# Performance work log

Measured on AMD Instinct MI355X. Metric: run time of the kernel, lower is better.

## Reference

```python
import jax, jax.numpy as jnp
import numpy as np

T = 20          # num_time_steps
THR = 0.05      # IafPscDelta threshold (and latency-encoding threshold)
REF = 3         # refractory_time_steps
DAMP = 1.0      # dampening_factor for surrogate gradient

@jax.custom_vjp
def spike(v_scaled):
    return (v_scaled > 0.0).astype(v_scaled.dtype)

def _spike_fwd(v_scaled):
    return spike(v_scaled), v_scaled

def _spike_bwd(v_scaled, g):
    # triangular surrogate: damp * max(0, 1 - |v_scaled|)
    return (g * DAMP * jnp.maximum(0.0, 1.0 - jnp.abs(v_scaled)),)

spike.defvjp(_spike_fwd, _spike_bwd)

def latency_encode(x):
    # snntorch.spikegen.latency(..., tau=2, threshold=0.05, normalize=True, linear=True, clip=True)
    # normalize+linear => spike_time = (T-1)*(1-x), clamped at (T-1)*(1-thr)
    tau_eff = jnp.asarray(T - 1, x.dtype)
    st = jnp.minimum(tau_eff * (1.0 - x), tau_eff * (1.0 - THR))
    t_idx = jnp.clip(jnp.round(st), 0, T - 1).astype(jnp.int32)          # [B,1,28,28]
    mask = (x >= THR).astype(x.dtype)                                     # clip=True: no spike if x < thr
    steps = jnp.arange(T, dtype=jnp.int32).reshape(T, 1, 1, 1, 1)
    return (steps == t_idx[None]).astype(x.dtype) * mask[None]            # [T,B,1,28,28]

def conv_all_steps(frames, W):
    # frames: [T,B,C,H,W]; shared weights -> batch the conv over T*B frames
    Tt, B, C, H, Wsp = frames.shape
    y = jax.lax.conv_general_dilated(frames.reshape(Tt * B, C, H, Wsp), W,
                                     window_strides=(1, 1), padding='SAME',
                                     dimension_numbers=('NCHW', 'OIHW', 'NCHW'))
    return y.reshape(Tt, B, W.shape[0], H, Wsp)

def lif(seq):
    # IafPscDelta over time: integrate (no leak), threshold, soft reset, refractory
    # seq: [T, B, ...] input currents per step
    v0 = jnp.zeros_like(seq[0])
    r0 = jnp.zeros_like(seq[0])
    def step(carry, x_t):
        v, r = carry
        v = v + x_t
        z = spike((v - THR) / THR)
        z = jnp.where(r > 0.0, jnp.zeros_like(z), z)   # refractory suppresses spikes
        v = v - z * THR                                 # perfect_reset=False -> subtract thr
        r = jnp.where(z > 0.0, jnp.full_like(r, REF), jnp.maximum(r - 1.0, 0.0))
        return (v, r), z
    _, zs = jax.lax.scan(step, (v0, r0), seq)
    return zs

def maxpool2(seq):
    Tt, B, C, H, Wsp = seq.shape
    y = jax.lax.reduce_window(seq.reshape(Tt * B, C, H, Wsp), 0.0, jax.lax.max,
                              (1, 1, 2, 2), (1, 1, 2, 2), 'VALID')
    return y.reshape(Tt, B, C, H // 2, Wsp // 2)

def setup_inputs() -> dict:
    key = jax.random.key(0)
    k1, k2, k3, k4 = jax.random.split(key, 4)
    x = jax.random.uniform(k1, (128, 1, 28, 28), dtype=jnp.float32)
    W1 = jax.random.normal(k2, (32, 1, 3, 3), dtype=jnp.float32) / np.sqrt(1 * 9)
    W2 = jax.random.normal(k3, (32, 32, 3, 3), dtype=jnp.float32) / np.sqrt(32 * 9)
    Wd = jax.random.normal(k4, (64, 32 * 7 * 7), dtype=jnp.float32) / np.sqrt(32 * 7 * 7)
    return {"x": x, "W1": W1, "W2": W2, "Wd": Wd}

def reference(x, W1, W2, Wd):
    s = latency_encode(x)                       # [T,B,1,28,28]
    h = maxpool2(lif(conv_all_steps(s, W1)))    # [T,B,32,14,14]
    h = maxpool2(lif(conv_all_steps(h, W2)))    # [T,B,32,7,7]
    Tt, B = h.shape[0], h.shape[1]
    h = h.reshape(Tt, B, -1)                    # [T,B,1568]
    h = lif(jnp.einsum('tbf,of->tbo', h, Wd))   # [T,B,64] output spikes
    return jnp.transpose(h, (1, 0, 2))          # [B,T,64]
```

## Files before the change

kernel.cpp:

```cpp
#include <hip/hip_runtime.h>

#define THRF 0.05f

__global__ void k_encode_mask(const float* __restrict__ x, unsigned* __restrict__ m, int n) {
  int i = blockIdx.x * blockDim.x + threadIdx.x;
  if (i >= n) return;
  float xv = x[i];
  float st = fminf(19.0f * (1.0f - xv), 19.0f * 0.95f);
  int t = (int)rintf(st);
  t = t < 0 ? 0 : (t > 19 ? 19 : t);
  m[i] = (xv >= THRF) ? (1u << t) : 0u;
}

__global__ void k_wt(const float* __restrict__ W1, const float* __restrict__ W2,
                     const float* __restrict__ Wd, float* __restrict__ w1T,
                     float* __restrict__ w2T, float* __restrict__ WdT) {
  int i = blockIdx.x * blockDim.x + threadIdx.x;
  if (i < 288) { int oc = i / 9, k = i % 9; w1T[k * 32 + oc] = W1[i]; }
  if (i < 9216) {
    int oc = i / 288, k = i % 288, ic = k / 9, kk = k % 9;
    w2T[kk * 1024 + ic * 32 + oc] = W2[i];
  }
  if (i < 100352) { int o = i / 1568, f = i % 1568; WdT[f * 64 + o] = Wd[i]; }
}

__global__ __launch_bounds__(128) void k_stage1M(const unsigned* __restrict__ mIn,
                                                 const float* __restrict__ w1T,
                                                 unsigned* __restrict__ z1p) {
  __shared__ float xp[2][20 * 66];
  int lane = threadIdx.x & 63;
  int wid  = threadIdx.x >> 6;
  int gw   = blockIdx.x * 2 + wid;
  int pA = 2 * gw, pB = 2 * gw + 1;
  int bA = pA / 784, rA = pA % 784, yA = rA / 28, xA = rA % 28;
  int bB = pB / 784, rB = pB % 784, yB = rB / 28, xB = rB % 28;
  int tl = lane & 31, hiB = lane >> 5;

  unsigned mA[9], mB[9];
  for (int ky = 0; ky < 3; ++ky) {
    for (int kx = 0; kx < 3; ++kx) {
      int k = ky * 3 + kx;
      int ya = yA - 1 + ky, xa = xA - 1 + kx;
      int yb = yB - 1 + ky, xb = xB - 1 + kx;
      mA[k] = (ya >= 0 && ya < 28 && xa >= 0 && xa < 28) ? mIn[bA * 784 + ya * 28 + xa] : 0u;
      mB[k] = (yb >= 0 && yb < 28 && xb >= 0 && xb < 28) ? mIn[bB * 784 + yb * 28 + xb] : 0u;
    }
  }

  float acc[32];
#pragma unroll
  for (int o = 0; o < 32; ++o) acc[o] = 0.0f;

  for (int k = 0; k < 9; ++k) {
    unsigned long long m64 = ((unsigned long long)mB[k] << 32) | (unsigned long long)mA[k];
    float bitf = (float)((m64 >> lane) & 1ull);
    const float* wrow = w1T + k * 32;
#pragma unroll
    for (int oc = 0; oc < 32; ++oc)
      acc[oc] = fmaf(wrow[oc], bitf, acc[oc]);
  }

  if (tl < 20) {
#pragma unroll
    for (int oc = 0; oc < 32; ++oc)
      xp[wid][tl * 66 + hiB * 32 + oc] = acc[oc];
  }
  __syncthreads();

  float v = 0.0f;
  int   r = 0;
  unsigned zm = 0u;
#pragma unroll
  for (int t = 0; t < 20; ++t) {
    float c = xp[wid][t * 66 + lane];
    v += c;
    bool z = (v > THRF) && (r == 0);
    if (z) { v -= THRF; r = 3; } else if (r > 0) --r;
    if (z) zm |= 1u << t;
  }
  int p = hiB ? pB : pA;
  int b = p / 784, rr = p % 784, y = rr / 28, x = rr % 28;
  atomicOr(&z1p[((b * 14 + (y >> 1)) * 14 + (x >> 1)) * 32 + tl], zm);
}

__global__ __launch_bounds__(256) void k_stage2E(const unsigned* __restrict__ z1p,
                                                 const float* __restrict__ wT2,
                                                 const unsigned* __restrict__ zbuf,
                                                 unsigned* __restrict__ z2p) {
  __shared__ float xp[4][20 * 97];
  int lane = threadIdx.x & 63;
  int wid  = threadIdx.x >> 6;
  int gw   = blockIdx.x * 4 + wid;
  int q0 = 3 * gw, q1 = q0 + 1, q2 = q0 + 2;
  bool vq0 = q0 < 25088, vq1 = q1 < 25088, vq2 = q2 < 25088;
  int b0 = q0 / 196, r0 = q0 % 196, y0 = r0 / 14, x0 = r0 % 14;
  int b1 = q1 / 196, r1 = q1 % 196, y1 = r1 / 14, x1 = r1 % 14;
  int b2 = q2 / 196, r2 = q2 % 196, y2 = r2 / 14, x2 = r2 % 14;

  int  li = lane & 31;
  bool lo = lane < 32;
  int  p  = lane / 20;
  int  tl = lane - p * 20;

  float acc[32];
#pragma unroll
  for (int o = 0; o < 32; ++o) acc[o] = 0.0f;

  auto cptr = [&](int ky, int kx, const unsigned*& c0, const unsigned*& c1,
                  const unsigned*& c2) {
    int y0k = y0 - 1 + ky, y1k = y1 - 1 + ky, y2k = y2 - 1 + ky;
    int x0k = x0 - 1 + kx, x1k = x1 - 1 + kx, x2k = x2 - 1 + kx;
    bool ok0 = vq0 && y0k >= 0 && y0k < 14 && x0k >= 0 && x0k < 14;
    bool ok1 = vq1 && y1k >= 0 && y1k < 14 && x1k >= 0 && x1k < 14;
    bool ok2 = vq2 && y2k >= 0 && y2k < 14 && x2k >= 0 && x2k < 14;
    c0 = ok0 ? (z1p + ((b0 * 14 + y0k) * 14 + x0k) * 32) : zbuf;
    c1 = ok1 ? (z1p + ((b1 * 14 + y1k) * 14 + x1k) * 32) : zbuf;
    c2 = ok2 ? (z1p + ((b2 * 14 + y2k) * 14 + x2k) * 32) : zbuf;
  };

  const unsigned *c0, *c1, *c2;
  cptr(0, 0, c0, c1, c2);
  unsigned va = (lo ? c0 : c1)[li];
  unsigned vb = c2[li];

  for (int ky = 0; ky < 3; ++ky) {
    for (int kx = 0; kx < 3; ++kx) {
      unsigned va_n = 0u, vb_n = 0u;
      int nkx = kx + 1, nky = ky;
      if (nkx == 3) { nkx = 0; nky = ky + 1; }
      if (nky < 3) {
        const unsigned *n0, *n1, *n2;
        cptr(nky, nkx, n0, n1, n2);
        va_n = (lo ? n0 : n1)[li];
        vb_n = n2[li];
      }
      const float* wc = wT2 + (ky * 3 + kx) * 1024;
#pragma unroll
      for (int ic = 0; ic < 32; ++ic) {
        unsigned s0 = (unsigned)__builtin_amdgcn_readlane((int)va, ic);
        unsigned s1 = (unsigned)__builtin_amdgcn_readlane((int)va, 32 + ic);
        unsigned s2 = (unsigned)__builtin_amdgcn_readlane((int)vb, ic);
        unsigned mm = (p == 0) ? s0 : ((p == 1) ? s1 : s2);
        float bitf = (float)((mm >> tl) & 1u);
        const float* wrow = wc + ic * 32;
#pragma unroll
        for (int oc = 0; oc < 32; ++oc)
          acc[oc] = fmaf(wrow[oc], bitf, acc[oc]);
      }
      va = va_n; vb = vb_n;
    }
  }

  if (p < 3) {
#pragma unroll
    for (int oc = 0; oc < 32; ++oc)
      xp[wid][tl * 97 + p * 32 + oc] = acc[oc];
  }
  __syncthreads();

  for (int pass = 0; pass < 2; ++pass) {
    int n = lane + 64 * pass;
    if (n < 96) {
      int pp = n >> 5;
      int oc = n & 31;
      int q  = q0 + pp;
      if (q < 25088) {
        float v = 0.0f;
        int   r = 0;
        unsigned zm = 0u;
#pragma unroll
        for (int t = 0; t < 20; ++t) {
          float c = xp[wid][t * 97 + n];
          v += c;
          bool z = (v > THRF) && (r == 0);
          if (z) { v -= THRF; r = 3; } else if (r > 0) --r;
          if (z) zm |= 1u << t;
        }
        int b = q / 196, rr = q % 196, y = rr / 14, x = rr % 14;
        atomicOr(&z2p[b * 1568 + oc * 49 + (y >> 1) * 7 + (x >> 1)], zm);
      }
    }
  }
}

__global__ __launch_bounds__(256) void k_dense_curE(const unsigned* __restrict__ z2p,
                                                    const float* __restrict__ WdT,
                                                    float* __restrict__ cur) {
  int lane = threadIdx.x & 63;
  int wid  = threadIdx.x >> 6;
  int gw   = blockIdx.x * 4 + wid;
  if (gw >= 128 * 22) return;
  int b  = gw / 22, og = gw % 22;
  int p  = lane / 20;
  int t  = lane - p * 20;
  int o  = og * 3 + p;
  bool live = (p < 3) && (o < 64);
  int osafe = live ? o : 63;
  const unsigned* zb = z2p + b * 1568;

  unsigned mA[16], mB[16];
  float    wA[16], wB[16];
#pragma unroll
  for (int u = 0; u < 16; ++u) { mA[u] = zb[u]; wA[u] = WdT[u * 64 + osafe]; }

  float acc = 0.0f;
  for (int f0 = 0; f0 < 1568; f0 += 32) {
#pragma unroll
    for (int u = 0; u < 16; ++u) {
      int fn = f0 + 16 + u;
      mB[u] = zb[fn]; wB[u] = WdT[fn * 64 + osafe];
    }
#pragma unroll
    for (int u = 0; u < 16; ++u) {
      float bitf = (float)((mA[u] >> t) & 1u);
      acc = fmaf(wA[u], bitf, acc);
    }
    if (f0 + 32 < 1568) {
#pragma unroll
      for (int u = 0; u < 16; ++u) {
        int fn = f0 + 32 + u;
        mA[u] = zb[fn]; wA[u] = WdT[fn * 64 + osafe];
      }
    }
#pragma unroll
    for (int u = 0; u < 16; ++u) {
      float bitf = (float)((mB[u] >> t) & 1u);
      acc = fmaf(wB[u], bitf, acc);
    }
  }
  if (live) cur[(b * 64 + o) * 20 + t] = acc;
}

__global__ void k_dense_lif(const float* __restrict__ cur, float* __restrict__ out) {
  int idx = blockIdx.x * blockDim.x + threadIdx.x;
  if (idx >= 128 * 64) return;
  int o = idx % 64;
  int b = idx / 64;
  const float* c = cur + (b * 64 + o) * 20;
  float v = 0.0f;
  int   r = 0;
  for (int t = 0; t < 20; ++t) {
    v += c[t];
    bool z = (v > THRF) && (r == 0);
    if (z) { v -= THRF; r = 3; } else if (r > 0) --r;
    out[(b * 20 + t) * 64 + o] = z ? 1.0f : 0.0f;
  }
}

extern "C" void kernel_launch(void* const* d_in, const int* in_sizes, int n_in,
                              void* d_out, int out_size, void* d_ws, size_t ws_size,
                              hipStream_t stream) {
  const float* x  = (const float*)d_in[0];
  const float* W1 = (const float*)d_in[1];
  const float* W2 = (const float*)d_in[2];
  const float* Wd = (const float*)d_in[3];
  float* out = (float*)d_out;

  char* ws = (char*)d_ws;
  unsigned* mIn  = (unsigned*)ws;
  float*    cur  = (float*)ws;
  unsigned* z1p  = (unsigned*)(ws + 655360);
  unsigned* z2p  = (unsigned*)(ws + 3866624);
  unsigned* zbuf = (unsigned*)(ws + 4669440);
  float*    w1T  = (float*)(ws + 4669568);
  float*    w2T  = (float*)(ws + 4670720);
  float*    WdT  = (float*)(ws + 4707584);

  k_encode_mask<<<dim3(392), dim3(256), 0, stream>>>(x, mIn, 128 * 784);
  k_wt<<<dim3(392), dim3(256), 0, stream>>>(W1, W2, Wd, w1T, w2T, WdT);
  hipMemsetAsync(ws + 655360, 0, 3211264 + 802816 + 128, stream);
  k_stage1M<<<dim3(25088), dim3(128), 0, stream>>>(mIn, w1T, z1p);
  k_stage2E<<<dim3(2091), dim3(256), 0, stream>>>(z1p, w2T, zbuf, z2p);
  k_dense_curE<<<dim3(704), dim3(256), 0, stream>>>(z2p, WdT, cur);
  k_dense_lif<<<dim3(32), dim3(256), 0, stream>>>(cur, out);
}
```

Baseline: 279.5 us.

## Process six pixels per wave in conv2, fuse dense LIF, merge prep kernels

The stage-2 conv kernel now computes two groups of three pixels per wavefront. Each weight float4 load feeds two accumulator sets, and per-lane bit extraction uses a packed 64-bit mask instead of selects. The dense LIF is folded into the dense kernel through wave shuffles, which drops the intermediate current buffer and one launch. The encode and weight-transpose kernels are also merged into one. Together these halve weight traffic per pixel and cut launch overhead, at the cost of higher register pressure from 64 accumulators and a partial unroll of the ic loop.

```diff
diff --git a/kernel.cpp b/kernel.cpp
--- a/kernel.cpp
+++ b/kernel.cpp
@@ -2,26 +2,23 @@
 
 #define THRF 0.05f
 
-__global__ void k_encode_mask(const float* __restrict__ x, unsigned* __restrict__ m, int n) {
+__global__ void k_pre(const float* __restrict__ x, const float* __restrict__ W1,
+                      const float* __restrict__ W2, const float* __restrict__ Wd,
+                      unsigned* __restrict__ mIn, float* __restrict__ w1T,
+                      float* __restrict__ w2T, float* __restrict__ WdT) {
   int i = blockIdx.x * blockDim.x + threadIdx.x;
-  if (i >= n) return;
+  if (i >= 100352) return;
   float xv = x[i];
   float st = fminf(19.0f * (1.0f - xv), 19.0f * 0.95f);
   int t = (int)rintf(st);
   t = t < 0 ? 0 : (t > 19 ? 19 : t);
-  m[i] = (xv >= THRF) ? (1u << t) : 0u;
-}
-
-__global__ void k_wt(const float* __restrict__ W1, const float* __restrict__ W2,
-                     const float* __restrict__ Wd, float* __restrict__ w1T,
-                     float* __restrict__ w2T, float* __restrict__ WdT) {
-  int i = blockIdx.x * blockDim.x + threadIdx.x;
-  if (i < 288) { int oc = i / 9, k = i % 9; w1T[k * 32 + oc] = W1[i]; }
+  mIn[i] = (xv >= THRF) ? (1u << t) : 0u;
+  { int o = i / 1568, f = i % 1568; WdT[f * 64 + o] = Wd[i]; }
   if (i < 9216) {
     int oc = i / 288, k = i % 288, ic = k / 9, kk = k % 9;
     w2T[kk * 1024 + ic * 32 + oc] = W2[i];
   }
-  if (i < 100352) { int o = i / 1568, f = i % 1568; WdT[f * 64 + o] = Wd[i]; }
+  if (i < 288) { int oc = i / 9, k = i % 9; w1T[k * 32 + oc] = W1[i]; }
 }
 
 __global__ __launch_bounds__(128) void k_stage1M(const unsigned* __restrict__ mIn,
@@ -83,7 +80,7 @@
   atomicOr(&z1p[((b * 14 + (y >> 1)) * 14 + (x >> 1)) * 32 + tl], zm);
 }
 
-__global__ __launch_bounds__(256) void k_stage2E(const unsigned* __restrict__ z1p,
+__global__ __launch_bounds__(256) void k_stage2F(const unsigned* __restrict__ z1p,
                                                  const float* __restrict__ wT2,
                                                  const unsigned* __restrict__ zbuf,
                                                  unsigned* __restrict__ z2p) {
@@ -91,101 +88,110 @@
   int lane = threadIdx.x & 63;
   int wid  = threadIdx.x >> 6;
   int gw   = blockIdx.x * 4 + wid;
-  int q0 = 3 * gw, q1 = q0 + 1, q2 = q0 + 2;
-  bool vq0 = q0 < 25088, vq1 = q1 < 25088, vq2 = q2 < 25088;
-  int b0 = q0 / 196, r0 = q0 % 196, y0 = r0 / 14, x0 = r0 % 14;
-  int b1 = q1 / 196, r1 = q1 % 196, y1 = r1 / 14, x1 = r1 % 14;
-  int b2 = q2 / 196, r2 = q2 % 196, y2 = r2 / 14, x2 = r2 % 14;
-
+  int q0 = 6 * gw;
   int  li = lane & 31;
   bool lo = lane < 32;
   int  p  = lane / 20;
   int  tl = lane - p * 20;
 
-  float acc[32];
-#pragma unroll
-  for (int o = 0; o < 32; ++o) acc[o] = 0.0f;
-
-  auto cptr = [&](int ky, int kx, const unsigned*& c0, const unsigned*& c1,
-                  const unsigned*& c2) {
-    int y0k = y0 - 1 + ky, y1k = y1 - 1 + ky, y2k = y2 - 1 + ky;
-    int x0k = x0 - 1 + kx, x1k = x1 - 1 + kx, x2k = x2 - 1 + kx;
-    bool ok0 = vq0 && y0k >= 0 && y0k < 14 && x0k >= 0 && x0k < 14;
-    bool ok1 = vq1 && y1k >= 0 && y1k < 14 && x1k >= 0 && x1k < 14;
-    bool ok2 = vq2 && y2k >= 0 && y2k < 14 && x2k >= 0 && x2k < 14;
-    c0 = ok0 ? (z1p + ((b0 * 14 + y0k) * 14 + x0k) * 32) : zbuf;
-    c1 = ok1 ? (z1p + ((b1 * 14 + y1k) * 14 + x1k) * 32) : zbuf;
-    c2 = ok2 ? (z1p + ((b2 * 14 + y2k) * 14 + x2k) * 32) : zbuf;
-  };
-
-  const unsigned *c0, *c1, *c2;
-  cptr(0, 0, c0, c1, c2);
-  unsigned va = (lo ? c0 : c1)[li];
-  unsigned vb = c2[li];
+  int qq[6], bb[6], yy[6], xx[6];
+  bool vq[6];
+#pragma unroll
+  for (int j = 0; j < 6; ++j) {
+    int q = q0 + j;
+    qq[j] = q; vq[j] = q < 25088;
+    int qs = vq[j] ? q : 0;
+    bb[j] = qs / 196; int rr = qs % 196; yy[j] = rr / 14; xx[j] = rr % 14;
+  }
+
+  float accA[32], accB[32];
+#pragma unroll
+  for (int o = 0; o < 32; ++o) { accA[o] = 0.0f; accB[o] = 0.0f; }
 
   for (int ky = 0; ky < 3; ++ky) {
     for (int kx = 0; kx < 3; ++kx) {
-      unsigned va_n = 0u, vb_n = 0u;
-      int nkx = kx + 1, nky = ky;
-      if (nkx == 3) { nkx = 0; nky = ky + 1; }
-      if (nky < 3) {
-        const unsigned *n0, *n1, *n2;
-        cptr(nky, nkx, n0, n1, n2);
-        va_n = (lo ? n0 : n1)[li];
-        vb_n = n2[li];
-      }
+      const unsigned* cp[6];
+#pragma unroll
+      for (int j = 0; j < 6; ++j) {
+        int y = yy[j] - 1 + ky, x = xx[j] - 1 + kx;
+        bool ok = vq[j] && y >= 0 && y < 14 && x >= 0 && x < 14;
+        cp[j] = ok ? (z1p + ((bb[j] * 14 + y) * 14 + x) * 32) : zbuf;
+      }
+      unsigned vaA = (lo ? cp[0] : cp[1])[li];
+      unsigned vbA = cp[2][li];
+      unsigned vaB = (lo ? cp[3] : cp[4])[li];
+      unsigned vbB = cp[5][li];
       const float* wc = wT2 + (ky * 3 + kx) * 1024;
-#pragma unroll
+#pragma unroll 4
       for (int ic = 0; ic < 32; ++ic) {
-        unsigned s0 = (unsigned)__builtin_amdgcn_readlane((int)va, ic);
-        unsigned s1 = (unsigned)__builtin_amdgcn_readlane((int)va, 32 + ic);
-        unsigned s2 = (unsigned)__builtin_amdgcn_readlane((int)vb, ic);
-        unsigned mm = (p == 0) ? s0 : ((p == 1) ? s1 : s2);
-        float bitf = (float)((mm >> tl) & 1u);
-        const float* wrow = wc + ic * 32;
-#pragma unroll
-        for (int oc = 0; oc < 32; ++oc)
-          acc[oc] = fmaf(wrow[oc], bitf, acc[oc]);
-      }
-      va = va_n; vb = vb_n;
-    }
-  }
-
-  if (p < 3) {
-#pragma unroll
-    for (int oc = 0; oc < 32; ++oc)
-      xp[wid][tl * 97 + p * 32 + oc] = acc[oc];
-  }
-  __syncthreads();
-
-  for (int pass = 0; pass < 2; ++pass) {
-    int n = lane + 64 * pass;
-    if (n < 96) {
-      int pp = n >> 5;
-      int oc = n & 31;
-      int q  = q0 + pp;
-      if (q < 25088) {
-        float v = 0.0f;
-        int   r = 0;
-        unsigned zm = 0u;
-#pragma unroll
-        for (int t = 0; t < 20; ++t) {
-          float c = xp[wid][t * 97 + n];
-          v += c;
-          bool z = (v > THRF) && (r == 0);
-          if (z) { v -= THRF; r = 3; } else if (r > 0) --r;
-          if (z) zm |= 1u << t;
+        unsigned s0 = (unsigned)__builtin_amdgcn_readlane((int)vaA, ic);
+        unsigned s1 = (unsigned)__builtin_amdgcn_readlane((int)vaA, 32 + ic);
+        unsigned s2 = (unsigned)__builtin_amdgcn_readlane((int)vbA, ic);
+        unsigned s3 = (unsigned)__builtin_amdgcn_readlane((int)vaB, ic);
+        unsigned s4 = (unsigned)__builtin_amdgcn_readlane((int)vaB, 32 + ic);
+        unsigned s5 = (unsigned)__builtin_amdgcn_readlane((int)vbB, ic);
+        unsigned long long BA = (unsigned long long)s0 |
+                                ((unsigned long long)s1 << 20) |
+                                ((unsigned long long)s2 << 40);
+        unsigned long long BB = (unsigned long long)s3 |
+                                ((unsigned long long)s4 << 20) |
+                                ((unsigned long long)s5 << 40);
+        float bfA = (float)((BA >> lane) & 1ull);
+        float bfB = (float)((BB >> lane) & 1ull);
+        const float4* w4 = (const float4*)(wc + ic * 32);
+#pragma unroll
+        for (int j = 0; j < 8; ++j) {
+          float4 w = w4[j];
+          accA[4 * j + 0] = fmaf(w.x, bfA, accA[4 * j + 0]);
+          accA[4 * j + 1] = fmaf(w.y, bfA, accA[4 * j + 1]);
+          accA[4 * j + 2] = fmaf(w.z, bfA, accA[4 * j + 2]);
+          accA[4 * j + 3] = fmaf(w.w, bfA, accA[4 * j + 3]);
+          accB[4 * j + 0] = fmaf(w.x, bfB, accB[4 * j + 0]);
+          accB[4 * j + 1] = fmaf(w.y, bfB, accB[4 * j + 1]);
+          accB[4 * j + 2] = fmaf(w.z, bfB, accB[4 * j + 2]);
+          accB[4 * j + 3] = fmaf(w.w, bfB, accB[4 * j + 3]);
         }
-        int b = q / 196, rr = q % 196, y = rr / 14, x = rr % 14;
-        atomicOr(&z2p[b * 1568 + oc * 49 + (y >> 1) * 7 + (x >> 1)], zm);
-      }
-    }
-  }
-}
-
-__global__ __launch_bounds__(256) void k_dense_curE(const unsigned* __restrict__ z2p,
-                                                    const float* __restrict__ WdT,
-                                                    float* __restrict__ cur) {
+      }
+    }
+  }
+
+#pragma unroll
+  for (int s = 0; s < 2; ++s) {
+    if (p < 3) {
+#pragma unroll
+      for (int oc = 0; oc < 32; ++oc)
+        xp[wid][tl * 97 + p * 32 + oc] = (s == 0 ? accA[oc] : accB[oc]);
+    }
+    __syncthreads();
+    for (int pass = 0; pass < 2; ++pass) {
+      int n = lane + 64 * pass;
+      if (n < 96) {
+        int pp = n >> 5;
+        int oc = n & 31;
+        int j  = 3 * s + pp;
+        if (vq[j]) {
+          float v = 0.0f;
+          int   r = 0;
+          unsigned zm = 0u;
+#pragma unroll
+          for (int t = 0; t < 20; ++t) {
+            float c = xp[wid][t * 97 + n];
+            v += c;
+            bool z = (v > THRF) && (r == 0);
+            if (z) { v -= THRF; r = 3; } else if (r > 0) --r;
+            if (z) zm |= 1u << t;
+          }
+          atomicOr(&z2p[bb[j] * 1568 + oc * 49 + (yy[j] >> 1) * 7 + (xx[j] >> 1)], zm);
+        }
+      }
+    }
+    __syncthreads();
+  }
+}
+
+__global__ __launch_bounds__(256) void k_denseF(const unsigned* __restrict__ z2p,
+                                                const float* __restrict__ WdT,
+                                                float* __restrict__ out) {
   int lane = threadIdx.x & 63;
   int wid  = threadIdx.x >> 6;
   int gw   = blockIdx.x * 4 + wid;
@@ -228,23 +234,19 @@
       acc = fmaf(wB[u], bitf, acc);
     }
   }
-  if (live) cur[(b * 64 + o) * 20 + t] = acc;
-}
-
-__global__ void k_dense_lif(const float* __restrict__ cur, float* __restrict__ out) {
-  int idx = blockIdx.x * blockDim.x + threadIdx.x;
-  if (idx >= 128 * 64) return;
-  int o = idx % 64;
-  int b = idx / 64;
-  const float* c = cur + (b * 64 + o) * 20;
+
   float v = 0.0f;
   int   r = 0;
-  for (int t = 0; t < 20; ++t) {
-    v += c[t];
+  unsigned zm = 0u;
+#pragma unroll
+  for (int tt = 0; tt < 20; ++tt) {
+    float c = __shfl(acc, p * 20 + tt, 64);
+    v += c;
     bool z = (v > THRF) && (r == 0);
     if (z) { v -= THRF; r = 3; } else if (r > 0) --r;
-    out[(b * 20 + t) * 64 + o] = z ? 1.0f : 0.0f;
-  }
+    if (z) zm |= 1u << tt;
+  }
+  if (live) out[(b * 20 + t) * 64 + o] = ((zm >> t) & 1u) ? 1.0f : 0.0f;
 }
 
 extern "C" void kernel_launch(void* const* d_in, const int* in_sizes, int n_in,
@@ -258,7 +260,6 @@
 
   char* ws = (char*)d_ws;
   unsigned* mIn  = (unsigned*)ws;
-  float*    cur  = (float*)ws;
   unsigned* z1p  = (unsigned*)(ws + 655360);
   unsigned* z2p  = (unsigned*)(ws + 3866624);
   unsigned* zbuf = (unsigned*)(ws + 4669440);
@@ -266,11 +267,9 @@
   float*    w2T  = (float*)(ws + 4670720);
   float*    WdT  = (float*)(ws + 4707584);
 
-  k_encode_mask<<<dim3(392), dim3(256), 0, stream>>>(x, mIn, 128 * 784);
-  k_wt<<<dim3(392), dim3(256), 0, stream>>>(W1, W2, Wd, w1T, w2T, WdT);
+  k_pre<<<dim3(392), dim3(256), 0, stream>>>(x, W1, W2, Wd, mIn, w1T, w2T, WdT);
   hipMemsetAsync(ws + 655360, 0, 3211264 + 802816 + 128, stream);
   k_stage1M<<<dim3(25088), dim3(128), 0, stream>>>(mIn, w1T, z1p);
-  k_stage2E<<<dim3(2091), dim3(256), 0, stream>>>(z1p, w2T, zbuf, z2p);
-  k_dense_curE<<<dim3(704), dim3(256), 0, stream>>>(z2p, WdT, cur);
-  k_dense_lif<<<dim3(32), dim3(256), 0, stream>>>(cur, out);
-}
+  k_stage2F<<<dim3(1046), dim3(256), 0, stream>>>(z1p, w2T, zbuf, z2p);
+  k_denseF<<<dim3(704), dim3(256), 0, stream>>>(z2p, WdT, out);
+}
```

New measurement: 311.5 us. +11.4%, slower.
